# Optimization experiments

Measured on AMD Instinct MI355X. Metric: run time of the kernel, lower is better.

Reference implementation:

```python
import jax, jax.numpy as jnp
import numpy as np

B = 4
N_PER_B = 65536
N = B * N_PER_B
GROUP_SIZE = 64
ORDER = 9  # min bits to cover grid size 512
C0, C1, C2 = 64, 128, 128


def hilbert_encode(coors, order):
    """Skilling AxesToTranspose, vectorized over N points, 3 dims -> int32 code."""
    n = 3
    X = [coors[:, i].astype(jnp.int32) for i in range(n)]
    M = 1 << (order - 1)
    Q = M
    while Q > 1:
        P = Q - 1
        for i in range(n):
            cond = (X[i] & Q) != 0
            if i == 0:
                X[0] = jnp.where(cond, X[0] ^ P, X[0])
            else:
                t = (X[0] ^ X[i]) & P
                x0 = jnp.where(cond, X[0] ^ P, X[0] ^ t)
                xi = jnp.where(cond, X[i], X[i] ^ t)
                X[0], X[i] = x0, xi
        Q >>= 1
    for i in range(1, n):
        X[i] = X[i] ^ X[i - 1]
    t = jnp.zeros_like(X[0])
    Q = M
    while Q > 1:
        t = jnp.where((X[n - 1] & Q) != 0, t ^ (Q - 1), t)
        Q >>= 1
    X = [x ^ t for x in X]
    # interleave transposed bits MSB-first: code has 3*order bits (27 < 31, fits int32)
    code = jnp.zeros_like(X[0])
    for b in range(order - 1, -1, -1):
        for i in range(n):
            code = (code << 1) | ((X[i] >> b) & 1)
    return code


def _mapping_indices(vox_coors):
    """Two Hilbert orderings (normal + reversed coord axes); per-batch stable grouping."""
    batch = vox_coors[:, 0]
    c1 = vox_coors[:, 1:4]
    c2 = vox_coors[:, 3:0:-1]  # [0,3,2,1] reverse of the xyz columns
    code1 = hilbert_encode(c1, ORDER)
    code2 = hilbert_encode(c2, ORDER)
    ind1 = jnp.lexsort((code1, batch))  # batch-major, curve-order minor
    ind2 = jnp.lexsort((code2, batch))
    inv1 = jnp.argsort(ind1)
    ind12 = inv1[ind2]  # maps ordering-1 arrangement to ordering-2 arrangement
    return ind1, ind12


def _block(p, x, params):
    """VoxFormer-style block: center pts per group, pos-encode, gate feats, local attn, FFN."""
    Wpos, bpos, Wq, Wk, Wv, Wo, Wout = params
    C = Wq.shape[0]
    gs = GROUP_SIZE
    pg = p.reshape(-1, gs, 3)
    e = (pg - pg.mean(axis=1, keepdims=True)).reshape(-1, 3) @ Wpos + bpos  # [N,C]
    h = (x * e).reshape(-1, gs, C)  # [G,gs,C]
    q, k, v = h @ Wq, h @ Wk, h @ Wv
    scores = jnp.einsum('gqc,gkc->gqk', q, k) / jnp.sqrt(jnp.asarray(C, q.dtype))
    attn = jax.nn.softmax(scores, axis=-1)
    o = jnp.einsum('gqk,gkc->gqc', attn, v).reshape(-1, C) @ Wo
    return jax.nn.relu(o) @ Wout  # [N,C_out]


def setup_inputs() -> dict:
    key = jax.random.key(0)
    ks = jax.random.split(key, 20)
    bcol = jnp.repeat(jnp.arange(B, dtype=jnp.int32), N_PER_B)
    z = jax.random.randint(ks[0], (N,), 0, 64, dtype=jnp.int32)
    y = jax.random.randint(ks[1], (N,), 0, 512, dtype=jnp.int32)
    x = jax.random.randint(ks[2], (N,), 0, 512, dtype=jnp.int32)
    vox_coors = jnp.stack([bcol, z, y, x], axis=1)
    vox_numbs = jnp.full((B,), N_PER_B, dtype=jnp.int32)
    vox_feats = jax.random.normal(ks[3], (N, C0), dtype=jnp.float32)
    pts_coors = jax.random.normal(ks[4], (N, 3), dtype=jnp.float32)
    s = lambda k, shape: jax.random.normal(k, shape, dtype=jnp.float32) / np.float32(np.sqrt(shape[0]))
    return dict(
        vox_numbs=vox_numbs, vox_coors=vox_coors, vox_feats=vox_feats, pts_coors=pts_coors,
        Wpos1=s(ks[5], (3, C0)), bpos1=jnp.zeros((C0,), jnp.float32),
        Wq1=s(ks[6], (C0, C0)), Wk1=s(ks[7], (C0, C0)), Wv1=s(ks[8], (C0, C0)),
        Wo1=s(ks[9], (C0, C0)), Wout1=s(ks[10], (C0, C1)),
        Wpos2=s(ks[11], (3, C1)), bpos2=jnp.zeros((C1,), jnp.float32),
        Wq2=s(ks[12], (C1, C1)), Wk2=s(ks[13], (C1, C1)), Wv2=s(ks[14], (C1, C1)),
        Wo2=s(ks[15], (C1, C1)), Wout2=s(ks[16], (C1, C2)),
    )


def reference(vox_numbs, vox_coors, vox_feats, pts_coors,
              Wpos1, bpos1, Wq1, Wk1, Wv1, Wo1, Wout1,
              Wpos2, bpos2, Wq2, Wk2, Wv2, Wo2, Wout2):
    ind1, ind12 = _mapping_indices(vox_coors)
    params = ((Wpos1, bpos1, Wq1, Wk1, Wv1, Wo1, Wout1),
              (Wpos2, bpos2, Wq2, Wk2, Wv2, Wo2, Wout2))
    for ind, prm in zip((ind1, ind12), params):
        vox_feats = vox_feats[ind]
        pts_coors = pts_coors[ind]
        vox_coors = vox_coors[ind]
        vox_feats = _block(pts_coors, vox_feats, prm)
    return vox_feats, pts_coors, vox_coors, vox_numbs
```

## Files before the change

### kernel.cpp

```cpp
#include <hip/hip_runtime.h>

using u64 = unsigned long long;
typedef _Float16 f16;
using f16x8 = __attribute__((ext_vector_type(8))) _Float16;
using f16x4 = __attribute__((ext_vector_type(4))) _Float16;
using f32x4 = __attribute__((ext_vector_type(4))) float;

__device__ __forceinline__ int hilbert3(int X0, int X1, int X2) {
  #pragma unroll
  for (int Q = 256; Q > 1; Q >>= 1) {
    const int P = Q - 1;
    if (X0 & Q) X0 ^= P;
    int t1 = (X0 ^ X1) & P;
    if (X1 & Q) X0 ^= P; else { X0 ^= t1; X1 ^= t1; }
    int t2 = (X0 ^ X2) & P;
    if (X2 & Q) X0 ^= P; else { X0 ^= t2; X2 ^= t2; }
  }
  X1 ^= X0;
  X2 ^= X1;
  int t = 0;
  #pragma unroll
  for (int Q = 256; Q > 1; Q >>= 1) if (X2 & Q) t ^= (Q - 1);
  X0 ^= t; X1 ^= t; X2 ^= t;
  int code = 0;
  #pragma unroll
  for (int b = 8; b >= 0; b--)
    code = (code << 3) | (((X0 >> b) & 1) << 2) | (((X1 >> b) & 1) << 1) | ((X2 >> b) & 1);
  return code;
}

__device__ __forceinline__ void cswap(u64& a, u64& b, bool up) {
  if ((a > b) == up) { u64 t = a; a = b; b = t; }
}

__global__ __launch_bounds__(1024) void sort_tile0(const int* __restrict__ vox,
                                                   u64* __restrict__ keys, int n,
                                                   int spanm1) {
  __shared__ u64 s[4096];
  const int base = blockIdx.x * 4096;
  const int bl = base & spanm1;
  #pragma unroll
  for (int m = 0; m < 4; m++) {
    const int e = base + threadIdx.x + m * 1024;
    const int isrc = e & (n - 1);
    const int4 c = ((const int4*)vox)[isrc];
    const unsigned code = (e < n) ? (unsigned)hilbert3(c.y, c.z, c.w)
                                  : (unsigned)hilbert3(c.w, c.z, c.y);
    s[threadIdx.x + m * 1024] =
        ((u64)(unsigned)c.x << 45) | ((u64)code << 18) | (unsigned)isrc;
  }
  __syncthreads();
  for (int k = 2; k <= 4096; k <<= 1) {
    for (int j = k >> 1; j >= 1; j >>= 1) {
      #pragma unroll
      for (int m = 0; m < 2; m++) {
        const int p = threadIdx.x + m * 1024;
        const int i = ((p & ~(j - 1)) << 1) | (p & (j - 1));
        const bool up = (((bl + i) & k) == 0);
        u64 a = s[i], b = s[i | j];
        if ((a > b) == up) { s[i] = b; s[i | j] = a; }
      }
      __syncthreads();
    }
  }
  #pragma unroll
  for (int m = 0; m < 4; m++)
    keys[base + threadIdx.x + m * 1024] = s[threadIdx.x + m * 1024];
}

template<int LEV>
__device__ __forceinline__ void gstepT(u64* __restrict__ keys, int t, int jlow,
                                       int k, int spanm1) {
  constexpr int S = 1 << LEV;
  const int i0 = ((t & ~(jlow - 1)) << LEV) | (t & (jlow - 1));
  const bool up = (((i0 & spanm1) & k) == 0);
  u64 x[S];
  #pragma unroll
  for (int m = 0; m < S; m++) x[m] = keys[i0 + (size_t)m * jlow];
  #pragma unroll
  for (int d = S >> 1; d >= 1; d >>= 1)
    #pragma unroll
    for (int m = 0; m < S; m++)
      if (!(m & d)) cswap(x[m], x[m | d], up);
  #pragma unroll
  for (int m = 0; m < S; m++) keys[i0 + (size_t)m * jlow] = x[m];
}

__global__ void bitonic_gN(u64* __restrict__ keys, int jlow, int lev, int k, int spanm1) {
  const int t = blockIdx.x * blockDim.x + threadIdx.x;
  switch (lev) {
    case 1: gstepT<1>(keys, t, jlow, k, spanm1); break;
    case 2: gstepT<2>(keys, t, jlow, k, spanm1); break;
    case 3: gstepT<3>(keys, t, jlow, k, spanm1); break;
    default: gstepT<4>(keys, t, jlow, k, spanm1); break;
  }
}

__global__ __launch_bounds__(1024) void merge_tile4(u64* __restrict__ keys, int k,
                                                    int spanm1) {
  __shared__ u64 s[4096];
  const int base = blockIdx.x * 4096;
  #pragma unroll
  for (int m = 0; m < 4; m++)
    s[threadIdx.x + m * 1024] = keys[base + threadIdx.x + m * 1024];
  __syncthreads();
  const bool up = (((base & spanm1) & k) == 0);
  for (int j = 2048; j >= 1; j >>= 1) {
    #pragma unroll
    for (int m = 0; m < 2; m++) {
      const int p = threadIdx.x + m * 1024;
      const int i = ((p & ~(j - 1)) << 1) | (p & (j - 1));
      u64 a = s[i], b = s[i | j];
      if ((a > b) == up) { s[i] = b; s[i | j] = a; }
    }
    __syncthreads();
  }
  #pragma unroll
  for (int m = 0; m < 4; m++)
    keys[base + threadIdx.x + m * 1024] = s[threadIdx.x + m * 1024];
}

__global__ void extract_inv_k(const u64* __restrict__ keys, const float* __restrict__ pts,
                              int* __restrict__ ind, int* __restrict__ inv,
                              float* __restrict__ pts1p, int n) {
  int t = blockIdx.x * blockDim.x + threadIdx.x;
  if (t >= n) return;
  int s = (int)(keys[t] & 0x3FFFFULL);
  ind[t] = s;
  inv[s] = t;
  pts1p[t * 3 + 0] = pts[s * 3 + 0];
  pts1p[t * 3 + 1] = pts[s * 3 + 1];
  pts1p[t * 3 + 2] = pts[s * 3 + 2];
}

__global__ void finish_k(const u64* __restrict__ keys2, const int* __restrict__ inv1,
                         int* __restrict__ g2, const float* __restrict__ pts,
                         const int* __restrict__ vox, const int* __restrict__ numbs,
                         float* __restrict__ out_pts, float* __restrict__ out_vox,
                         float* __restrict__ out_nb, int n, int B) {
  int t = blockIdx.x * blockDim.x + threadIdx.x;
  if (t >= n) return;
  int s = (int)(keys2[t] & 0x3FFFFULL);
  g2[t] = inv1[s];
  out_pts[t * 3 + 0] = pts[s * 3 + 0];
  out_pts[t * 3 + 1] = pts[s * 3 + 1];
  out_pts[t * 3 + 2] = pts[s * 3 + 2];
  const int4 v = ((const int4*)vox)[s];
  out_vox[t * 4 + 0] = (float)v.x;
  out_vox[t * 4 + 1] = (float)v.y;
  out_vox[t * 4 + 2] = (float)v.z;
  out_vox[t * 4 + 3] = (float)v.w;
  if (t < B) out_nb[t] = (float)numbs[t];
}

__global__ void prep_all(const float* __restrict__ Wq1, const float* __restrict__ Wk1,
                         const float* __restrict__ Wv1, const float* __restrict__ Wo1,
                         const float* __restrict__ Wout1,
                         const float* __restrict__ Wq2, const float* __restrict__ Wk2,
                         const float* __restrict__ Wv2, const float* __restrict__ Wo2,
                         const float* __restrict__ Wout2,
                         f16* __restrict__ A1a, f16* __restrict__ A2a, f16* __restrict__ A3a,
                         f16* __restrict__ A1b, f16* __restrict__ A2b, f16* __restrict__ A3b) {
  const int idx = blockIdx.x * blockDim.x + threadIdx.x;
  if (idx < 4096) {
    const int a = idx >> 6, b = idx & 63;
    float s1 = 0.f, s2 = 0.f;
    for (int c = 0; c < 64; c++) {
      s1 = fmaf(Wq1[b * 64 + c], Wk1[a * 64 + c], s1);
      s2 = fmaf(Wv1[b * 64 + c], Wo1[c * 64 + a], s2);
    }
    A1a[idx] = (f16)(s1 * 0.125f);
    A2a[idx] = (f16)s2;
  }
  if (idx < 8192) {
    const int o = idx >> 6, c = idx & 63;
    A3a[idx] = (f16)Wout1[c * 128 + o];
  }
  {
    const int a = idx >> 7, b = idx & 127;
    float s1 = 0.f, s2 = 0.f;
    for (int c = 0; c < 128; c++) {
      s1 = fmaf(Wq2[b * 128 + c], Wk2[a * 128 + c], s1);
      s2 = fmaf(Wv2[b * 128 + c], Wo2[c * 128 + a], s2);
    }
    A1b[idx] = (f16)(s1 * 0.08838834764831845f);
    A2b[idx] = (f16)s2;
    A3b[idx] = (f16)Wout2[b * 128 + a];
  }
}

__device__ __forceinline__ int swzb(int row) { return ((row ^ (row >> 3)) & 7) << 4; }

template<int M, int K, int AMODE>
__device__ __forceinline__ void gemmT(const f16* __restrict__ Ag, const f16* __restrict__ lA,
                                      const f16* __restrict__ lB, int w, int lane,
                                      f32x4 (&acc)[M / 64][4]) {
  constexpr int CT = M / 64;
  const int lr = lane & 15, lk = lane >> 4;
  #pragma unroll
  for (int ks = 0; ks < K / 32; ks++) {
    const int k0 = ks * 32 + lk * 8;
    f16x8 Af[CT];
    #pragma unroll
    for (int ct = 0; ct < CT; ct++) {
      const int c = lr + (w * CT + ct) * 16;
      if (AMODE == 0) {
        Af[ct] = *(const f16x8*)(Ag + (size_t)c * K + k0);
      } else if (AMODE == 1) {
        Af[ct] = *(const f16x8*)((const char*)lA + (((c * K + k0) * 2) ^ swzb(c)));
      } else {
        f16x8 a;
        #pragma unroll
        for (int e = 0; e < 8; e++) {
          const int j = k0 + e;
          a[e] = *(const f16*)((const char*)lA + (((j * M + c) * 2) ^ swzb(j)));
        }
        Af[ct] = a;
      }
    }
    f16x8 Bf[4];
    #pragma unroll
    for (int qt = 0; qt < 4; qt++) {
      const int q = lr + qt * 16;
      Bf[qt] = *(const f16x8*)((const char*)lB + (((q * K + k0) * 2) ^ swzb(q)));
    }
    #pragma unroll
    for (int ct = 0; ct < CT; ct++)
      #pragma unroll
      for (int qt = 0; qt < 4; qt++)
        acc[ct][qt] = __builtin_amdgcn_mfma_f32_16x16x32_f16(Af[ct], Bf[qt], acc[ct][qt], 0, 0, 0);
  }
}

template<int M, bool RELU>
__device__ __forceinline__ void storeT16(f16* __restrict__ dst, int w, int lane,
                                         const f32x4 (&acc)[M / 64][4]) {
  constexpr int CT = M / 64;
  #pragma unroll
  for (int ct = 0; ct < CT; ct++)
    #pragma unroll
    for (int qt = 0; qt < 4; qt++) {
      const int q = (lane & 15) + qt * 16;
      const int c0 = (w * CT + ct) * 16 + (lane >> 4) * 4;
      f16x4 v;
      #pragma unroll
      for (int r = 0; r < 4; r++) {
        float x = acc[ct][qt][r];
        if (RELU) x = fmaxf(x, 0.f);
        v[r] = (f16)x;
      }
      *(f16x4*)((char*)dst + (((q * M + c0) * 2) ^ swzb(q))) = v;
    }
}

template<int C, bool X16, bool OUT16>
__global__ __launch_bounds__(512, 4) void block_mfma(
    const int* __restrict__ idx_x, const float* __restrict__ ptsP,
    const void* __restrict__ xsrc,
    const float* __restrict__ Wpos, const float* __restrict__ bpos,
    const f16* __restrict__ A1, const f16* __restrict__ A2, const f16* __restrict__ A3,
    void* __restrict__ outp) {
  constexpr int CT = C / 64;
  constexpr int GSZ = 64 * C * 4 + 8192;
  extern __shared__ char smem_raw[];
  char* smem = smem_raw + (threadIdx.x >> 8) * GSZ;
  f16* bufH = (f16*)smem;
  f16* bufT = bufH + 64 * C;
  f16* scH  = bufT + 64 * C;

  const int g = blockIdx.x * 2 + (threadIdx.x >> 8);
  const int t = threadIdx.x & 255;
  const int lane = t & 63;
  const int w = t >> 6;
  const int lr = lane & 15, lk = lane >> 4;

  f16x8 A1f[C / 32][CT];
  #pragma unroll
  for (int ks = 0; ks < C / 32; ks++)
    #pragma unroll
    for (int ct = 0; ct < CT; ct++)
      A1f[ks][ct] = *(const f16x8*)(A1 + (size_t)(lr + (w * CT + ct) * 16) * C + ks * 32 + lk * 8);

  const int q = t >> 2, qq = t & 3;
  const int sx = idx_x[g * 64 + q];
  float xv[C / 4];
  if (X16) {
    #pragma unroll
    for (int i = 0; i < C / 32; i++) {
      f16x8 xr = *(const f16x8*)((const f16*)xsrc + (size_t)sx * C + qq * (C / 4) + i * 8);
      #pragma unroll
      for (int j = 0; j < 8; j++) xv[i * 8 + j] = (float)xr[j];
    }
  } else {
    #pragma unroll
    for (int i = 0; i < C / 16; i++) {
      float4 x0 = *(const float4*)((const float*)xsrc + (size_t)sx * C + qq * (C / 4) + i * 4);
      xv[i * 4 + 0] = x0.x; xv[i * 4 + 1] = x0.y; xv[i * 4 + 2] = x0.z; xv[i * 4 + 3] = x0.w;
    }
  }

  {
    float mx = ptsP[(g * 64 + lane) * 3 + 0];
    float my = ptsP[(g * 64 + lane) * 3 + 1];
    float mz = ptsP[(g * 64 + lane) * 3 + 2];
    #pragma unroll
    for (int o = 32; o > 0; o >>= 1) {
      mx += __shfl_xor(mx, o); my += __shfl_xor(my, o); mz += __shfl_xor(mz, o);
    }
    mx *= (1.f / 64.f); my *= (1.f / 64.f); mz *= (1.f / 64.f);

    const float d0 = ptsP[(g * 64 + q) * 3 + 0] - mx;
    const float d1 = ptsP[(g * 64 + q) * 3 + 1] - my;
    const float d2 = ptsP[(g * 64 + q) * 3 + 2] - mz;
    #pragma unroll
    for (int i = 0; i < C / 32; i++) {
      const int c0 = qq * (C / 4) + i * 8;
      f16x8 hv;
      #pragma unroll
      for (int jj = 0; jj < 8; jj += 4) {
        const float4 w0 = *(const float4*)(Wpos + 0 * C + c0 + jj);
        const float4 w1 = *(const float4*)(Wpos + 1 * C + c0 + jj);
        const float4 w2 = *(const float4*)(Wpos + 2 * C + c0 + jj);
        const float4 bb = *(const float4*)(bpos + c0 + jj);
        hv[jj + 0] = (f16)(xv[i * 8 + jj + 0] * fmaf(d0, w0.x, fmaf(d1, w1.x, fmaf(d2, w2.x, bb.x))));
        hv[jj + 1] = (f16)(xv[i * 8 + jj + 1] * fmaf(d0, w0.y, fmaf(d1, w1.y, fmaf(d2, w2.y, bb.y))));
        hv[jj + 2] = (f16)(xv[i * 8 + jj + 2] * fmaf(d0, w0.z, fmaf(d1, w1.z, fmaf(d2, w2.z, bb.z))));
        hv[jj + 3] = (f16)(xv[i * 8 + jj + 3] * fmaf(d0, w0.w, fmaf(d1, w1.w, fmaf(d2, w2.w, bb.w))));
      }
      *(f16x8*)((char*)bufH + (((q * C + c0) * 2) ^ swzb(q))) = hv;
    }
  }
  __syncthreads();

  {
    f32x4 acc[CT][4] = {};
    #pragma unroll
    for (int ks = 0; ks < C / 32; ks++) {
      const int k0 = ks * 32 + lk * 8;
      f16x8 Bf[4];
      #pragma unroll
      for (int qt = 0; qt < 4; qt++) {
        const int qr = lr + qt * 16;
        Bf[qt] = *(const f16x8*)((const char*)bufH + (((qr * C + k0) * 2) ^ swzb(qr)));
      }
      #pragma unroll
      for (int ct = 0; ct < CT; ct++)
        #pragma unroll
        for (int qt = 0; qt < 4; qt++)
          acc[ct][qt] = __builtin_amdgcn_mfma_f32_16x16x32_f16(A1f[ks][ct], Bf[qt], acc[ct][qt], 0, 0, 0);
    }
    storeT16<C, false>(bufT, w, lane, acc);
  }
  __syncthreads();

  {
    f32x4 acc[1][4] = {};
    gemmT<64, C, 1>(nullptr, bufH, bufT, w, lane, acc);
    #pragma unroll
    for (int qt = 0; qt < 4; qt++) {
      const int qr = lr + qt * 16;
      const int j0 = w * 16 + lk * 4;
      f16x4 v;
      #pragma unroll
      for (int r = 0; r < 4; r++) v[r] = (f16)acc[0][qt][r];
      *(f16x4*)((char*)scH + (((qr * 64 + j0) * 2) ^ swzb(qr))) = v;
    }
  }
  __syncthreads();

  {
    float v[16];
    float mxv = -3.0e38f;
    #pragma unroll
    for (int i = 0; i < 2; i++) {
      f16x8 x8 = *(const f16x8*)((const char*)scH + (((q * 64 + qq * 16 + i * 8) * 2) ^ swzb(q)));
      #pragma unroll
      for (int j = 0; j < 8; j++) {
        v[i * 8 + j] = (float)x8[j];
        mxv = fmaxf(mxv, v[i * 8 + j]);
      }
    }
    mxv = fmaxf(mxv, __shfl_xor(mxv, 1));
    mxv = fmaxf(mxv, __shfl_xor(mxv, 2));
    float s = 0.f;
    #pragma unroll
    for (int i = 0; i < 16; i++) { v[i] = __expf(v[i] - mxv); s += v[i]; }
    s += __shfl_xor(s, 1);
    s += __shfl_xor(s, 2);
    const float inv = 1.f / s;
    #pragma unroll
    for (int i = 0; i < 2; i++) {
      f16x8 pk;
      #pragma unroll
      for (int j = 0; j < 8; j++) pk[j] = (f16)(v[i * 8 + j] * inv);
      *(f16x8*)((char*)scH + (((q * 64 + qq * 16 + i * 8) * 2) ^ swzb(q))) = pk;
    }
  }
  __syncthreads();

  {
    f32x4 acc[CT][4] = {};
    gemmT<C, 64, 2>(nullptr, bufH, scH, w, lane, acc);
    storeT16<C, false>(bufT, w, lane, acc);
  }
  __syncthreads();

  {
    f32x4 acc[CT][4] = {};
    gemmT<C, C, 0>(A2, nullptr, bufT, w, lane, acc);
    storeT16<C, true>(bufH, w, lane, acc);
  }
  __syncthreads();

  {
    f32x4 acc[2][4] = {};
    gemmT<128, C, 0>(A3, nullptr, bufH, w, lane, acc);
    #pragma unroll
    for (int ct = 0; ct < 2; ct++)
      #pragma unroll
      for (int qt = 0; qt < 4; qt++) {
        const int qr = (lane & 15) + qt * 16;
        const int o0 = (w * 2 + ct) * 16 + (lane >> 4) * 4;
        const size_t row = (size_t)g * 64 + qr;
        if (OUT16) {
          f16x4 v;
          #pragma unroll
          for (int r = 0; r < 4; r++) v[r] = (f16)acc[ct][qt][r];
          *(f16x4*)((f16*)outp + row * 128 + o0) = v;
        } else {
          *(f32x4*)((float*)outp + row * 128 + o0) = acc[ct][qt];
        }
      }
  }
}

extern "C" void kernel_launch(void* const* d_in, const int* in_sizes, int n_in,
                              void* d_out, int out_size, void* d_ws, size_t ws_size,
                              hipStream_t stream) {
  const int*   vox_numbs = (const int*)d_in[0];
  const int*   vox_coors = (const int*)d_in[1];
  const float* vox_feats = (const float*)d_in[2];
  const float* pts_coors = (const float*)d_in[3];
  const float* Wpos1 = (const float*)d_in[4];
  const float* bpos1 = (const float*)d_in[5];
  const float* Wq1   = (const float*)d_in[6];
  const float* Wk1   = (const float*)d_in[7];
  const float* Wv1   = (const float*)d_in[8];
  const float* Wo1   = (const float*)d_in[9];
  const float* Wout1 = (const float*)d_in[10];
  const float* Wpos2 = (const float*)d_in[11];
  const float* bpos2 = (const float*)d_in[12];
  const float* Wq2   = (const float*)d_in[13];
  const float* Wk2   = (const float*)d_in[14];
  const float* Wv2   = (const float*)d_in[15];
  const float* Wo2   = (const float*)d_in[16];
  const float* Wout2 = (const float*)d_in[17];

  const int B = in_sizes[0];
  const int n = in_sizes[1] / 4;
  const int ngrp = n / 64;

  char* w = (char*)d_ws;
  auto alloc = [&](size_t bytes) {
    char* p = w;
    w += (bytes + 255) & ~(size_t)255;
    return p;
  };
  u64* keys    = (u64*)alloc((size_t)2 * n * 8);
  int* ind1    = (int*)alloc((size_t)n * 4);
  int* inv1    = (int*)alloc((size_t)n * 4);
  int* g2      = (int*)alloc((size_t)n * 4);
  float* pts1p = (float*)alloc((size_t)n * 3 * 4);
  f16* A1a     = (f16*)alloc(64 * 64 * 2);
  f16* A2a     = (f16*)alloc(64 * 64 * 2);
  f16* A3a     = (f16*)alloc(128 * 64 * 2);
  f16* A1b     = (f16*)alloc(128 * 128 * 2);
  f16* A2b     = (f16*)alloc(128 * 128 * 2);
  f16* A3b     = (f16*)alloc(128 * 128 * 2);
  f16* feats1  = (f16*)alloc((size_t)n * 128 * 2);
  u64* keys2   = keys + n;

  float* out_feats = (float*)d_out;
  float* out_pts   = out_feats + (size_t)n * 128;
  float* out_vox   = out_pts + (size_t)n * 3;
  float* out_nb    = out_vox + (size_t)n * 4;

  auto f64k  = block_mfma<64,  false, true>;
  auto f128k = block_mfma<128, true,  false>;
  hipFuncSetAttribute((const void*)f64k,  hipFuncAttributeMaxDynamicSharedMemorySize, 65536);
  hipFuncSetAttribute((const void*)f128k, hipFuncAttributeMaxDynamicSharedMemorySize, 98304);

  prep_all<<<64, 256, 0, stream>>>(Wq1, Wk1, Wv1, Wo1, Wout1, Wq2, Wk2, Wv2, Wo2, Wout2,
                                   A1a, A2a, A3a, A1b, A2b, A3b);

  int span = (B > 0) ? n / B : n;
  if (span < 8192 || (span & (span - 1)) != 0 || n % span != 0) span = n;
  const int spanm1 = span - 1;

  sort_tile0<<<2 * n / 4096, 1024, 0, stream>>>(vox_coors, keys, n, spanm1);
  for (int k = 8192; k <= span; k <<= 1) {
    int j = k >> 1;
    while (j >= 4096) {
      int lev = 1;
      while (lev < 4 && (j >> lev) >= 4096) lev++;
      const int jlow = j >> (lev - 1);
      const int nth = (2 * n) >> lev;
      bitonic_gN<<<nth / 256, 256, 0, stream>>>(keys, jlow, lev, k, spanm1);
      j = jlow >> 1;
    }
    merge_tile4<<<2 * n / 4096, 1024, 0, stream>>>(keys, k, spanm1);
  }

  extract_inv_k<<<(n + 255) / 256, 256, 0, stream>>>(keys, pts_coors, ind1, inv1, pts1p, n);
  finish_k<<<(n + 255) / 256, 256, 0, stream>>>(keys2, inv1, g2, pts_coors, vox_coors,
                                                vox_numbs, out_pts, out_vox, out_nb, n, B);

  block_mfma<64, false, true><<<ngrp / 2, 512, 2 * 24576, stream>>>(
      ind1, pts1p, vox_feats, Wpos1, bpos1, A1a, A2a, A3a, feats1);
  block_mfma<128, true, false><<<ngrp / 2, 512, 2 * 40960, stream>>>(
      g2, out_pts, feats1, Wpos2, bpos2, A1b, A2b, A3b, out_feats);
}
```

Before: 305.9 us.

## Use one group per 512-thread block with 8 waves splitting each MFMA stage

Each block of 512 threads used to process two 64-point groups with four waves per group; now one group is spread over eight waves, and every GEMM stage splits its output tiles across the eight waves. Each wave keeps its A fragments for all K steps in registers and reloads B per tile. The LDS swizzle changes, launch bounds rise to 8 blocks per CU, and shared memory per block is halved. The aim is to cut per-wave register pressure and raise occupancy and latency hiding, at the cost of twice as many blocks and more barrier syncs per unit of work.

```diff
diff --git a/kernel.cpp b/kernel.cpp
--- a/kernel.cpp
+++ b/kernel.cpp
@@ -189,117 +189,90 @@
   }
 }
 
-__device__ __forceinline__ int swzb(int row) { return ((row ^ (row >> 3)) & 7) << 4; }
+__device__ __forceinline__ int swzb(int row) {
+  return (((row & 7) ^ (((row >> 3) & 3) << 1)) << 4);
+}
 
 template<int M, int K, int AMODE>
-__device__ __forceinline__ void gemmT(const f16* __restrict__ Ag, const f16* __restrict__ lA,
-                                      const f16* __restrict__ lB, int w, int lane,
-                                      f32x4 (&acc)[M / 64][4]) {
-  constexpr int CT = M / 64;
+__device__ __forceinline__ void stage8(const f16* __restrict__ Ag,
+                                       const f16* __restrict__ lA,
+                                       const f16* __restrict__ lB,
+                                       int w, int lane,
+                                       f32x4 (&acc)[(M / 16) * 4 / 8]) {
+  constexpr int NPW = (M / 16) * 4 / 8;
+  constexpr int KT = K / 32;
   const int lr = lane & 15, lk = lane >> 4;
-  #pragma unroll
-  for (int ks = 0; ks < K / 32; ks++) {
-    const int k0 = ks * 32 + lk * 8;
-    f16x8 Af[CT];
-    #pragma unroll
-    for (int ct = 0; ct < CT; ct++) {
-      const int c = lr + (w * CT + ct) * 16;
-      if (AMODE == 0) {
-        Af[ct] = *(const f16x8*)(Ag + (size_t)c * K + k0);
-      } else if (AMODE == 1) {
-        Af[ct] = *(const f16x8*)((const char*)lA + (((c * K + k0) * 2) ^ swzb(c)));
-      } else {
-        f16x8 a;
-        #pragma unroll
-        for (int e = 0; e < 8; e++) {
-          const int j = k0 + e;
-          a[e] = *(const f16*)((const char*)lA + (((j * M + c) * 2) ^ swzb(j)));
-        }
-        Af[ct] = a;
+  const int ct = (w * NPW) >> 2;
+  const int qt0 = (w * NPW) & 3;
+  const int c = ct * 16 + lr;
+  f16x8 Af[KT];
+  #pragma unroll
+  for (int kt = 0; kt < KT; kt++) {
+    const int k0 = kt * 32 + lk * 8;
+    if (AMODE == 0) {
+      Af[kt] = *(const f16x8*)(Ag + (size_t)c * K + k0);
+    } else if (AMODE == 1) {
+      Af[kt] = *(const f16x8*)((const char*)lA + (((c * K + k0) * 2) ^ swzb(c)));
+    } else {
+      f16x8 a;
+      #pragma unroll
+      for (int e = 0; e < 8; e++) {
+        const int j = k0 + e;
+        a[e] = *(const f16*)((const char*)lA + (((j * M + c) * 2) ^ swzb(j)));
       }
-    }
-    f16x8 Bf[4];
-    #pragma unroll
-    for (int qt = 0; qt < 4; qt++) {
-      const int q = lr + qt * 16;
-      Bf[qt] = *(const f16x8*)((const char*)lB + (((q * K + k0) * 2) ^ swzb(q)));
-    }
-    #pragma unroll
-    for (int ct = 0; ct < CT; ct++)
-      #pragma unroll
-      for (int qt = 0; qt < 4; qt++)
-        acc[ct][qt] = __builtin_amdgcn_mfma_f32_16x16x32_f16(Af[ct], Bf[qt], acc[ct][qt], 0, 0, 0);
-  }
-}
-
-template<int M, bool RELU>
-__device__ __forceinline__ void storeT16(f16* __restrict__ dst, int w, int lane,
-                                         const f32x4 (&acc)[M / 64][4]) {
-  constexpr int CT = M / 64;
-  #pragma unroll
-  for (int ct = 0; ct < CT; ct++)
-    #pragma unroll
-    for (int qt = 0; qt < 4; qt++) {
-      const int q = (lane & 15) + qt * 16;
-      const int c0 = (w * CT + ct) * 16 + (lane >> 4) * 4;
-      f16x4 v;
-      #pragma unroll
-      for (int r = 0; r < 4; r++) {
-        float x = acc[ct][qt][r];
-        if (RELU) x = fmaxf(x, 0.f);
-        v[r] = (f16)x;
-      }
-      *(f16x4*)((char*)dst + (((q * M + c0) * 2) ^ swzb(q))) = v;
-    }
+      Af[kt] = a;
+    }
+  }
+  #pragma unroll
+  for (int i = 0; i < NPW; i++) {
+    const int q = lr + (qt0 + i) * 16;
+    #pragma unroll
+    for (int kt = 0; kt < KT; kt++) {
+      const int k0 = kt * 32 + lk * 8;
+      const f16x8 Bf = *(const f16x8*)((const char*)lB + (((q * K + k0) * 2) ^ swzb(q)));
+      acc[i] = __builtin_amdgcn_mfma_f32_16x16x32_f16(Af[kt], Bf, acc[i], 0, 0, 0);
+    }
+  }
+}
+
+template<int RL, bool RELU>
+__device__ __forceinline__ void store8(f16* __restrict__ dst, int ct, int qt,
+                                       int lane, f32x4 v) {
+  const int lr = lane & 15, lk = lane >> 4;
+  const int q = lr + qt * 16;
+  const int c0 = ct * 16 + lk * 4;
+  f16x4 o;
+  #pragma unroll
+  for (int r = 0; r < 4; r++) {
+    float x = v[r];
+    if (RELU) x = fmaxf(x, 0.f);
+    o[r] = (f16)x;
+  }
+  *(f16x4*)((char*)dst + (((q * RL + c0) * 2) ^ swzb(q))) = o;
 }
 
 template<int C, bool X16, bool OUT16>
-__global__ __launch_bounds__(512, 4) void block_mfma(
+__global__ __launch_bounds__(512, 8) void block_mfma(
     const int* __restrict__ idx_x, const float* __restrict__ ptsP,
     const void* __restrict__ xsrc,
     const float* __restrict__ Wpos, const float* __restrict__ bpos,
     const f16* __restrict__ A1, const f16* __restrict__ A2, const f16* __restrict__ A3,
     void* __restrict__ outp) {
-  constexpr int CT = C / 64;
-  constexpr int GSZ = 64 * C * 4 + 8192;
-  extern __shared__ char smem_raw[];
-  char* smem = smem_raw + (threadIdx.x >> 8) * GSZ;
+  constexpr int NPWC = C / 32;
+  extern __shared__ char smem[];
   f16* bufH = (f16*)smem;
   f16* bufT = bufH + 64 * C;
   f16* scH  = bufT + 64 * C;
 
-  const int g = blockIdx.x * 2 + (threadIdx.x >> 8);
-  const int t = threadIdx.x & 255;
+  const int g = blockIdx.x;
+  const int t = threadIdx.x;
   const int lane = t & 63;
   const int w = t >> 6;
   const int lr = lane & 15, lk = lane >> 4;
-
-  f16x8 A1f[C / 32][CT];
-  #pragma unroll
-  for (int ks = 0; ks < C / 32; ks++)
-    #pragma unroll
-    for (int ct = 0; ct < CT; ct++)
-      A1f[ks][ct] = *(const f16x8*)(A1 + (size_t)(lr + (w * CT + ct) * 16) * C + ks * 32 + lk * 8);
-
-  const int q = t >> 2, qq = t & 3;
-  const int sx = idx_x[g * 64 + q];
-  float xv[C / 4];
-  if (X16) {
-    #pragma unroll
-    for (int i = 0; i < C / 32; i++) {
-      f16x8 xr = *(const f16x8*)((const f16*)xsrc + (size_t)sx * C + qq * (C / 4) + i * 8);
-      #pragma unroll
-      for (int j = 0; j < 8; j++) xv[i * 8 + j] = (float)xr[j];
-    }
-  } else {
-    #pragma unroll
-    for (int i = 0; i < C / 16; i++) {
-      float4 x0 = *(const float4*)((const float*)xsrc + (size_t)sx * C + qq * (C / 4) + i * 4);
-      xv[i * 4 + 0] = x0.x; xv[i * 4 + 1] = x0.y; xv[i * 4 + 2] = x0.z; xv[i * 4 + 3] = x0.w;
-    }
-  }
-
-  {
+  const int q8 = t >> 3, qq = t & 7;
+
+  {
+    const int sx = idx_x[g * 64 + q8];
     float mx = ptsP[(g * 64 + lane) * 3 + 0];
     float my = ptsP[(g * 64 + lane) * 3 + 1];
     float mz = ptsP[(g * 64 + lane) * 3 + 2];
@@ -308,13 +281,23 @@
       mx += __shfl_xor(mx, o); my += __shfl_xor(my, o); mz += __shfl_xor(mz, o);
     }
     mx *= (1.f / 64.f); my *= (1.f / 64.f); mz *= (1.f / 64.f);
-
-    const float d0 = ptsP[(g * 64 + q) * 3 + 0] - mx;
-    const float d1 = ptsP[(g * 64 + q) * 3 + 1] - my;
-    const float d2 = ptsP[(g * 64 + q) * 3 + 2] - mz;
-    #pragma unroll
-    for (int i = 0; i < C / 32; i++) {
-      const int c0 = qq * (C / 4) + i * 8;
+    const float d0 = ptsP[(g * 64 + q8) * 3 + 0] - mx;
+    const float d1 = ptsP[(g * 64 + q8) * 3 + 1] - my;
+    const float d2 = ptsP[(g * 64 + q8) * 3 + 2] - mz;
+    #pragma unroll
+    for (int i = 0; i < C / 64; i++) {
+      const int c0 = qq * (C / 8) + i * 8;
+      float xa[8];
+      if constexpr (X16) {
+        f16x8 xr = *(const f16x8*)((const f16*)xsrc + (size_t)sx * C + c0);
+        #pragma unroll
+        for (int j = 0; j < 8; j++) xa[j] = (float)xr[j];
+      } else {
+        float4 x0 = *(const float4*)((const float*)xsrc + (size_t)sx * C + c0);
+        float4 x1 = *(const float4*)((const float*)xsrc + (size_t)sx * C + c0 + 4);
+        xa[0] = x0.x; xa[1] = x0.y; xa[2] = x0.z; xa[3] = x0.w;
+        xa[4] = x1.x; xa[5] = x1.y; xa[6] = x1.z; xa[7] = x1.w;
+      }
       f16x8 hv;
       #pragma unroll
       for (int jj = 0; jj < 8; jj += 4) {
@@ -322,115 +305,95 @@
         const float4 w1 = *(const float4*)(Wpos + 1 * C + c0 + jj);
         const float4 w2 = *(const float4*)(Wpos + 2 * C + c0 + jj);
         const float4 bb = *(const float4*)(bpos + c0 + jj);
-        hv[jj + 0] = (f16)(xv[i * 8 + jj + 0] * fmaf(d0, w0.x, fmaf(d1, w1.x, fmaf(d2, w2.x, bb.x))));
-        hv[jj + 1] = (f16)(xv[i * 8 + jj + 1] * fmaf(d0, w0.y, fmaf(d1, w1.y, fmaf(d2, w2.y, bb.y))));
-        hv[jj + 2] = (f16)(xv[i * 8 + jj + 2] * fmaf(d0, w0.z, fmaf(d1, w1.z, fmaf(d2, w2.z, bb.z))));
-        hv[jj + 3] = (f16)(xv[i * 8 + jj + 3] * fmaf(d0, w0.w, fmaf(d1, w1.w, fmaf(d2, w2.w, bb.w))));
+        hv[jj + 0] = (f16)(xa[jj + 0] * fmaf(d0, w0.x, fmaf(d1, w1.x, fmaf(d2, w2.x, bb.x))));
+        hv[jj + 1] = (f16)(xa[jj + 1] * fmaf(d0, w0.y, fmaf(d1, w1.y, fmaf(d2, w2.y, bb.y))));
+        hv[jj + 2] = (f16)(xa[jj + 2] * fmaf(d0, w0.z, fmaf(d1, w1.z, fmaf(d2, w2.z, bb.z))));
+        hv[jj + 3] = (f16)(xa[jj + 3] * fmaf(d0, w0.w, fmaf(d1, w1.w, fmaf(d2, w2.w, bb.w))));
       }
-      *(f16x8*)((char*)bufH + (((q * C + c0) * 2) ^ swzb(q))) = hv;
-    }
-  }
-  __syncthreads();
-
-  {
-    f32x4 acc[CT][4] = {};
-    #pragma unroll
-    for (int ks = 0; ks < C / 32; ks++) {
-      const int k0 = ks * 32 + lk * 8;
-      f16x8 Bf[4];
-      #pragma unroll
-      for (int qt = 0; qt < 4; qt++) {
-        const int qr = lr + qt * 16;
-        Bf[qt] = *(const f16x8*)((const char*)bufH + (((qr * C + k0) * 2) ^ swzb(qr)));
-      }
-      #pragma unroll
-      for (int ct = 0; ct < CT; ct++)
-        #pragma unroll
-        for (int qt = 0; qt < 4; qt++)
-          acc[ct][qt] = __builtin_amdgcn_mfma_f32_16x16x32_f16(A1f[ks][ct], Bf[qt], acc[ct][qt], 0, 0, 0);
-    }
-    storeT16<C, false>(bufT, w, lane, acc);
-  }
-  __syncthreads();
-
-  {
-    f32x4 acc[1][4] = {};
-    gemmT<64, C, 1>(nullptr, bufH, bufT, w, lane, acc);
-    #pragma unroll
-    for (int qt = 0; qt < 4; qt++) {
-      const int qr = lr + qt * 16;
-      const int j0 = w * 16 + lk * 4;
-      f16x4 v;
-      #pragma unroll
-      for (int r = 0; r < 4; r++) v[r] = (f16)acc[0][qt][r];
-      *(f16x4*)((char*)scH + (((qr * 64 + j0) * 2) ^ swzb(qr))) = v;
-    }
-  }
-  __syncthreads();
-
-  {
-    float v[16];
+      *(f16x8*)((char*)bufH + (((q8 * C + c0) * 2) ^ swzb(q8))) = hv;
+    }
+  }
+  __syncthreads();
+
+  {
+    f32x4 acc[NPWC] = {};
+    stage8<C, C, 0>(A1, nullptr, bufH, w, lane, acc);
+    const int ct = (w * NPWC) >> 2, qt0 = (w * NPWC) & 3;
+    #pragma unroll
+    for (int i = 0; i < NPWC; i++) store8<C, false>(bufT, ct, qt0 + i, lane, acc[i]);
+  }
+  __syncthreads();
+
+  {
+    f32x4 acc[2] = {};
+    stage8<64, C, 1>(nullptr, bufH, bufT, w, lane, acc);
+    const int ct = (w * 2) >> 2, qt0 = (w * 2) & 3;
+    #pragma unroll
+    for (int i = 0; i < 2; i++) store8<64, false>(scH, ct, qt0 + i, lane, acc[i]);
+  }
+  __syncthreads();
+
+  {
+    f16x8 x8 = *(const f16x8*)((const char*)scH + (((q8 * 64 + qq * 8) * 2) ^ swzb(q8)));
+    float v[8];
     float mxv = -3.0e38f;
     #pragma unroll
-    for (int i = 0; i < 2; i++) {
-      f16x8 x8 = *(const f16x8*)((const char*)scH + (((q * 64 + qq * 16 + i * 8) * 2) ^ swzb(q)));
-      #pragma unroll
-      for (int j = 0; j < 8; j++) {
-        v[i * 8 + j] = (float)x8[j];
-        mxv = fmaxf(mxv, v[i * 8 + j]);
-      }
+    for (int j = 0; j < 8; j++) {
+      v[j] = (float)x8[j];
+      mxv = fmaxf(mxv, v[j]);
     }
     mxv = fmaxf(mxv, __shfl_xor(mxv, 1));
     mxv = fmaxf(mxv, __shfl_xor(mxv, 2));
+    mxv = fmaxf(mxv, __shfl_xor(mxv, 4));
     float s = 0.f;
     #pragma unroll
-    for (int i = 0; i < 16; i++) { v[i] = __expf(v[i] - mxv); s += v[i]; }
+    for (int j = 0; j < 8; j++) { v[j] = __expf(v[j] - mxv); s += v[j]; }
     s += __shfl_xor(s, 1);
     s += __shfl_xor(s, 2);
+    s += __shfl_xor(s, 4);
     const float inv = 1.f / s;
-    #pragma unroll
-    for (int i = 0; i < 2; i++) {
-      f16x8 pk;
-      #pragma unroll
-      for (int j = 0; j < 8; j++) pk[j] = (f16)(v[i * 8 + j] * inv);
-      *(f16x8*)((char*)scH + (((q * 64 + qq * 16 + i * 8) * 2) ^ swzb(q))) = pk;
-    }
-  }
-  __syncthreads();
-
-  {
-    f32x4 acc[CT][4] = {};
-    gemmT<C, 64, 2>(nullptr, bufH, scH, w, lane, acc);
-    storeT16<C, false>(bufT, w, lane, acc);
-  }
-  __syncthreads();
-
-  {
-    f32x4 acc[CT][4] = {};
-    gemmT<C, C, 0>(A2, nullptr, bufT, w, lane, acc);
-    storeT16<C, true>(bufH, w, lane, acc);
-  }
-  __syncthreads();
-
-  {
-    f32x4 acc[2][4] = {};
-    gemmT<128, C, 0>(A3, nullptr, bufH, w, lane, acc);
-    #pragma unroll
-    for (int ct = 0; ct < 2; ct++)
-      #pragma unroll
-      for (int qt = 0; qt < 4; qt++) {
-        const int qr = (lane & 15) + qt * 16;
-        const int o0 = (w * 2 + ct) * 16 + (lane >> 4) * 4;
-        const size_t row = (size_t)g * 64 + qr;
-        if (OUT16) {
-          f16x4 v;
-          #pragma unroll
-          for (int r = 0; r < 4; r++) v[r] = (f16)acc[ct][qt][r];
-          *(f16x4*)((f16*)outp + row * 128 + o0) = v;
-        } else {
-          *(f32x4*)((float*)outp + row * 128 + o0) = acc[ct][qt];
-        }
+    f16x8 pk;
+    #pragma unroll
+    for (int j = 0; j < 8; j++) pk[j] = (f16)(v[j] * inv);
+    *(f16x8*)((char*)scH + (((q8 * 64 + qq * 8) * 2) ^ swzb(q8))) = pk;
+  }
+  __syncthreads();
+
+  {
+    f32x4 acc[NPWC] = {};
+    stage8<C, 64, 2>(nullptr, bufH, scH, w, lane, acc);
+    const int ct = (w * NPWC) >> 2, qt0 = (w * NPWC) & 3;
+    #pragma unroll
+    for (int i = 0; i < NPWC; i++) store8<C, false>(bufT, ct, qt0 + i, lane, acc[i]);
+  }
+  __syncthreads();
+
+  {
+    f32x4 acc[NPWC] = {};
+    stage8<C, C, 0>(A2, nullptr, bufT, w, lane, acc);
+    const int ct = (w * NPWC) >> 2, qt0 = (w * NPWC) & 3;
+    #pragma unroll
+    for (int i = 0; i < NPWC; i++) store8<C, true>(bufH, ct, qt0 + i, lane, acc[i]);
+  }
+  __syncthreads();
+
+  {
+    f32x4 acc[4] = {};
+    stage8<128, C, 0>(A3, nullptr, bufH, w, lane, acc);
+    #pragma unroll
+    for (int i = 0; i < 4; i++) {
+      const int qr = lr + i * 16;
+      const int o0 = w * 16 + lk * 4;
+      const size_t row = (size_t)g * 64 + qr;
+      if (OUT16) {
+        f16x4 v;
+        #pragma unroll
+        for (int r = 0; r < 4; r++) v[r] = (f16)acc[i][r];
+        *(f16x4*)((f16*)outp + row * 128 + o0) = v;
+      } else {
+        *(f32x4*)((float*)outp + row * 128 + o0) = acc[i];
       }
+    }
   }
 }
 
@@ -488,7 +451,7 @@
   auto f64k  = block_mfma<64,  false, true>;
   auto f128k = block_mfma<128, true,  false>;
   hipFuncSetAttribute((const void*)f64k,  hipFuncAttributeMaxDynamicSharedMemorySize, 65536);
-  hipFuncSetAttribute((const void*)f128k, hipFuncAttributeMaxDynamicSharedMemorySize, 98304);
+  hipFuncSetAttribute((const void*)f128k, hipFuncAttributeMaxDynamicSharedMemorySize, 65536);
 
   prep_all<<<64, 256, 0, stream>>>(Wq1, Wk1, Wv1, Wo1, Wout1, Wq2, Wk2, Wv2, Wo2, Wout2,
                                    A1a, A2a, A3a, A1b, A2b, A3b);
@@ -515,8 +478,8 @@
   finish_k<<<(n + 255) / 256, 256, 0, stream>>>(keys2, inv1, g2, pts_coors, vox_coors,
                                                 vox_numbs, out_pts, out_vox, out_nb, n, B);
 
-  block_mfma<64, false, true><<<ngrp / 2, 512, 2 * 24576, stream>>>(
+  block_mfma<64, false, true><<<ngrp, 512, 24576, stream>>>(
       ind1, pts1p, vox_feats, Wpos1, bpos1, A1a, A2a, A3a, feats1);
-  block_mfma<128, true, false><<<ngrp / 2, 512, 2 * 40960, stream>>>(
+  block_mfma<128, true, false><<<ngrp, 512, 40960, stream>>>(
       g2, out_pts, feats1, Wpos2, bpos2, A1b, A2b, A3b, out_feats);
 }
```

Result: faster. 274.0 us (-10.4%).
